# Optimization experiments

Measured on AMD Instinct MI355X. Metric: run time of the kernel, lower is better.

The kernel has to match this reference:

```python
import jax, jax.numpy as jnp
import numpy as np

N_ATOMS = 300000
N_COLS = 8
VOCAB = 4096      # nn.Embedding(4096, per_col_dim)
D_COL = 32        # per_col_dim
HID = 256         # hidden_size
N_BONDS = 320000
B_GRAPHS = 6000
ATOMS_PER_GRAPH = 50
STEPS = 3
SENTINEL = 999999999


def _linear_params(key, fan_in, fan_out):
    lim = 1.0 / np.sqrt(fan_in)
    kw, kb = jax.random.split(key)
    W = jax.random.uniform(kw, (fan_out, fan_in), minval=-lim, maxval=lim, dtype=jnp.float32)
    b = jax.random.uniform(kb, (fan_out,), minval=-lim, maxval=lim, dtype=jnp.float32)
    return W, b


def setup_inputs() -> dict:
    key = jax.random.key(0)
    ks = jax.random.split(key, 8)
    a_features = jax.random.randint(ks[0], (N_ATOMS, N_COLS), 0, VOCAB, dtype=jnp.int32)
    uv = jax.random.randint(ks[1], (N_BONDS, 2), 0, N_ATOMS, dtype=jnp.int32)
    bextra = jax.random.randint(ks[2], (N_BONDS, 1), 0, 16, dtype=jnp.int32)
    b_features = jnp.concatenate([uv, bextra], axis=1)
    # contiguous equal-length scopes: graph i owns atoms [i*50, i*50+50)
    starts = np.arange(B_GRAPHS, dtype=np.int32) * ATOMS_PER_GRAPH
    lengths = np.full(B_GRAPHS, ATOMS_PER_GRAPH, dtype=np.int32)
    a_scopes = jnp.asarray(np.stack([starts, lengths], axis=1))
    emb_weights = jax.random.normal(ks[3], (N_COLS, VOCAB, D_COL), dtype=jnp.float32) * 0.02
    W_in, b_in = _linear_params(ks[4], D_COL, HID)
    W_self, b_self = _linear_params(ks[5], HID, HID)
    W_neigh, b_neigh = _linear_params(ks[6], HID, HID)
    W_out, b_out = _linear_params(ks[7], HID, HID)
    return {
        'a_features': a_features, 'b_features': b_features, 'a_scopes': a_scopes,
        'emb_weights': emb_weights,
        'W_in': W_in, 'b_in': b_in,
        'W_self': W_self, 'b_self': b_self,
        'W_neigh': W_neigh, 'b_neigh': b_neigh,
        'W_out': W_out, 'b_out': b_out,
    }


def reference(a_features, b_features, a_scopes, emb_weights,
              W_in, b_in, W_self, b_self, W_neigh, b_neigh, W_out, b_out):
    # --- per-column embedding lookup, summed over columns ---
    idx = jnp.remainder(a_features, VOCAB)
    idx = jnp.where(a_features >= SENTINEL, 0, idx)          # sentinel -> index 0
    x = jnp.zeros((a_features.shape[0], D_COL), dtype=emb_weights.dtype)
    for c in range(N_COLS):                                   # fixed small loop over columns
        x = x + emb_weights[c][idx[:, c]]
    h = x @ W_in.T + b_in                                     # [N, HID]
    # --- undirected edges -> two directed edge lists ---
    u = b_features[:, 0]
    v = b_features[:, 1]
    src = jnp.concatenate([u, v], axis=0)
    dst = jnp.concatenate([v, u], axis=0)
    # --- message passing steps ---
    for _ in range(STEPS):
        agg = jnp.zeros_like(h).at[dst].add(h[src])           # scatter-add neighbor sum
        h = jax.nn.relu(h @ W_self.T + b_self + agg @ W_neigh.T + b_neigh)
    h = h @ W_out.T + b_out
    # --- per-graph mean pooling over contiguous scopes ---
    lengths = a_scopes[:, 1]
    seg_ids = jnp.repeat(jnp.arange(a_scopes.shape[0]), lengths,
                         total_repeat_length=h.shape[0])
    sums = jax.ops.segment_sum(h, seg_ids, num_segments=a_scopes.shape[0])
    denom = jnp.maximum(lengths, 1).astype(h.dtype)[:, None]
    return sums / denom
```

## Files before the change

kernel.cpp:

```cpp
#include <hip/hip_runtime.h>

#define NATOMS 300000
#define NCOLS 8
#define VOCABSZ 4096
#define DCOL 32
#define HIDDIM 256
#define NBONDS 320000
#define NGRAPHS 6000
#define NSTEPS 3

constexpr int MP = 300032;
constexpr int MTILES128 = MP / 128;
constexpr int HSTR = 2 * HIDDIM;
constexpr int XSTR = 2 * DCOL;

typedef _Float16 f16;
typedef _Float16 f16x8 __attribute__((ext_vector_type(8)));
typedef float f32x4 __attribute__((ext_vector_type(4)));

constexpr float LO_SCALE = 2048.0f;
constexpr float INV_LO   = 1.0f / 2048.0f;

__device__ __forceinline__ void split2(float x, f16& h, f16& l) {
    h = (f16)x;
    l = (f16)((x - (float)h) * LO_SCALE);
}

__device__ __forceinline__ int swz(int row, int q) {
    return (row * 4 + (q ^ ((row >> 1) & 3))) * 8;
}

__device__ __forceinline__ void dma16(const f16* g, f16* l) {
    __builtin_amdgcn_global_load_lds(
        (const __attribute__((address_space(1))) uint32_t*)g,
        (__attribute__((address_space(3))) uint32_t*)l, 16, 0, 0);
}

static void* g_pool = nullptr;
__attribute__((constructor)) static void alloc_pool() {
    void* p = nullptr;
    if (hipMalloc(&p, (size_t)1024 * 1024 * 1024) == hipSuccess) {
        hipMemset(p, 0, (size_t)1024 * 1024 * 1024);
        g_pool = p;
    }
}

__global__ void fill_kernel(float* out, float v, int n) {
    int i = blockIdx.x * blockDim.x + threadIdx.x;
    if (i < n) out[i] = v;
}

__global__ void build_edges_kernel(const int* __restrict__ bf, int* __restrict__ esrc,
                                   int* __restrict__ nxt, int* head) {
    int e = blockIdx.x * blockDim.x + threadIdx.x;
    if (e >= 2 * NBONDS) return;
    int src, dst;
    if (e < NBONDS) { src = bf[e * 3 + 0]; dst = bf[e * 3 + 1]; }
    else { int i = e - NBONDS; src = bf[i * 3 + 1]; dst = bf[i * 3 + 0]; }
    esrc[e] = src;
    nxt[e] = atomicExch(&head[dst], e);
}

__global__ void wsplit_kernel(const float* __restrict__ W, f16* __restrict__ Wh,
                              f16* __restrict__ Wl, int n) {
    int i = blockIdx.x * blockDim.x + threadIdx.x;
    if (i >= n) return;
    split2(W[i], Wh[i], Wl[i]);
}

__global__ void bsum_kernel(const float* __restrict__ a, const float* __restrict__ b,
                            float* __restrict__ o) {
    int i = threadIdx.x;
    o[i] = a[i] + b[i];
}

__global__ void embed_kernel(const int* __restrict__ af, const float* __restrict__ emb,
                             f16* __restrict__ x) {
    int gid = blockIdx.x * blockDim.x + threadIdx.x;
    int i = gid >> 5, k = gid & 31;
    if (i >= NATOMS) return;
    float s = 0.0f;
#pragma unroll
    for (int c = 0; c < NCOLS; c++) {
        int v = af[i * NCOLS + c];
        int idx = v & (VOCABSZ - 1);
        if (v >= 999999999) idx = 0;
        s += emb[((size_t)c * VOCABSZ + idx) * DCOL + k];
    }
    f16 hi, lo;
    split2(s, hi, lo);
    x[(size_t)i * XSTR + k] = hi;
    x[(size_t)i * XSTR + DCOL + k] = lo;
}

__global__ void agg_kernel(const f16* __restrict__ H, f16* __restrict__ G,
                           const int* __restrict__ head, const int* __restrict__ nxt,
                           const int* __restrict__ esrc) {
    int wid = (blockIdx.x * blockDim.x + threadIdx.x) >> 6;
    int lane = threadIdx.x & 63;
    if (wid >= NATOMS) return;
    float a0 = 0.f, a1 = 0.f, a2 = 0.f, a3 = 0.f,
          a4 = 0.f, a5 = 0.f, a6 = 0.f, a7 = 0.f;
    int e = head[wid];
    while (e >= 0) {
        int src = esrc[e];
        const f16x8 v = *(const f16x8*)(H + (size_t)src * HSTR + lane * 8);
        a0 += (float)v[0]; a1 += (float)v[1]; a2 += (float)v[2]; a3 += (float)v[3];
        a4 += (float)v[4]; a5 += (float)v[5]; a6 += (float)v[6]; a7 += (float)v[7];
        e = nxt[e];
    }
    const bool isLo = lane >= 32;
    if (isLo) {
        a0 *= INV_LO; a1 *= INV_LO; a2 *= INV_LO; a3 *= INV_LO;
        a4 *= INV_LO; a5 *= INV_LO; a6 *= INV_LO; a7 *= INV_LO;
    }
    float s0 = a0 + __shfl_xor(a0, 32, 64);
    float s1 = a1 + __shfl_xor(a1, 32, 64);
    float s2 = a2 + __shfl_xor(a2, 32, 64);
    float s3 = a3 + __shfl_xor(a3, 32, 64);
    float s4 = a4 + __shfl_xor(a4, 32, 64);
    float s5 = a5 + __shfl_xor(a5, 32, 64);
    float s6 = a6 + __shfl_xor(a6, 32, 64);
    float s7 = a7 + __shfl_xor(a7, 32, 64);
    f16x8 o;
#define EMIT(J, S)                                                    \
    {                                                                 \
        const f16 hv = (f16)(S);                                      \
        o[J] = isLo ? (f16)(((S) - (float)hv) * LO_SCALE) : hv;       \
    }
    EMIT(0, s0) EMIT(1, s1) EMIT(2, s2) EMIT(3, s3)
    EMIT(4, s4) EMIT(5, s5) EMIT(6, s6) EMIT(7, s7)
#undef EMIT
    *(f16x8*)(G + (size_t)wid * HSTR + lane * 8) = o;
}

template <bool HAS_A2, bool RELU, int K>
__global__ __launch_bounds__(512, 2) void mfma_gemm(
    const f16* __restrict__ A1, const f16* __restrict__ A2,
    const f16* __restrict__ B1h, const f16* __restrict__ B1l,
    const f16* __restrict__ B2h, const f16* __restrict__ B2l,
    const float* __restrict__ bias, f16* __restrict__ C) {
    constexpr int OAH = 0, OAL = 4096, OBH = 8192, OBL = 16384, BUFH = 24576;
    __shared__ __align__(16) f16 lds[2 * BUFH];

    const int t = threadIdx.x;
    const int m0 = blockIdx.x * 128;
    const int lane = t & 63;
    const int wid = t >> 6;
    const int wr = wid >> 2;
    const int wc = wid & 3;
    const int quad = lane >> 4;
    const int l16 = lane & 15;

    const int ra_ = wid * 16 + (lane >> 2);
    const int qs_ = (lane & 3) ^ ((ra_ >> 1) & 3);
    const int ko_ = qs_ * 8;

    f32x4 acch[4][4], accl[4][4];
#pragma unroll
    for (int a = 0; a < 4; a++)
#pragma unroll
        for (int b = 0; b < 4; b++) {
            acch[a][b] = (f32x4){0.f, 0.f, 0.f, 0.f};
            accl[a][b] = (f32x4){0.f, 0.f, 0.f, 0.f};
        }

    constexpr int NMAT = HAS_A2 ? 2 : 1;
    constexpr int NST = (K / 32) * NMAT;

#define ISSUE_STAGE(S, BUF)                                                    \
    {                                                                          \
        const int mat_ = HAS_A2 ? ((S) & 1) : 0;                               \
        const int kb_ = (HAS_A2 ? ((S) >> 1) : (S)) * 32;                      \
        const f16* A_ = (mat_ == 0) ? A1 : A2;                                 \
        const f16* Bh_ = (mat_ == 0) ? B1h : B2h;                              \
        const f16* Bl_ = (mat_ == 0) ? B1l : B2l;                              \
        f16* const dst_ = lds + (BUF) * BUFH + wid * 512;                      \
        const size_t arow_ = (size_t)(m0 + ra_) * (2 * K) + kb_ + ko_;         \
        dma16(A_ + arow_, dst_ + OAH);                                         \
        dma16(A_ + arow_ + K, dst_ + OAL);                                     \
        const size_t brow_ = (size_t)ra_ * K + kb_ + ko_;                      \
        dma16(Bh_ + brow_, dst_ + OBH);                                        \
        dma16(Bh_ + brow_ + (size_t)128 * K, dst_ + OBH + 4096);               \
        dma16(Bl_ + brow_, dst_ + OBL);                                        \
        dma16(Bl_ + brow_ + (size_t)128 * K, dst_ + OBL + 4096);               \
    }

    ISSUE_STAGE(0, 0);

    for (int s = 0; s < NST; s++) {
        __syncthreads();
        if (s + 1 < NST) ISSUE_STAGE(s + 1, (s + 1) & 1);

        const f16* cb = lds + (s & 1) * BUFH;
        const f16* sAh = cb + OAH;
        const f16* sAl = cb + OAL;
        const f16* sBh = cb + OBH;
        const f16* sBl = cb + OBL;

        f16x8 fah[4], fal[4];
#pragma unroll
        for (int mt = 0; mt < 4; mt++) {
            const int src = swz(wr * 64 + mt * 16 + l16, quad);
            fah[mt] = *(const f16x8*)(sAh + src);
            fal[mt] = *(const f16x8*)(sAl + src);
        }
#pragma unroll
        for (int nt = 0; nt < 4; nt++) {
            const int src = swz(wc * 64 + nt * 16 + l16, quad);
            const f16x8 bh = *(const f16x8*)(sBh + src);
            const f16x8 bl = *(const f16x8*)(sBl + src);
#pragma unroll
            for (int mt = 0; mt < 4; mt++) {
                acch[mt][nt] = __builtin_amdgcn_mfma_f32_16x16x32_f16(fah[mt], bh, acch[mt][nt], 0, 0, 0);
                accl[mt][nt] = __builtin_amdgcn_mfma_f32_16x16x32_f16(fah[mt], bl, accl[mt][nt], 0, 0, 0);
                accl[mt][nt] = __builtin_amdgcn_mfma_f32_16x16x32_f16(fal[mt], bh, accl[mt][nt], 0, 0, 0);
            }
        }
    }
#undef ISSUE_STAGE

#pragma unroll
    for (int mt = 0; mt < 4; mt++) {
#pragma unroll
        for (int nt = 0; nt < 4; nt++) {
            const int col = wc * 64 + nt * 16 + l16;
            const float bv = bias[col];
#pragma unroll
            for (int r = 0; r < 4; r++) {
                const int row = m0 + wr * 64 + mt * 16 + quad * 4 + r;
                float v = acch[mt][nt][r] + accl[mt][nt][r] * INV_LO + bv;
                if (RELU) v = fmaxf(v, 0.f);
                f16 hi, lo;
                split2(v, hi, lo);
                C[(size_t)row * HSTR + col] = hi;
                C[(size_t)row * HSTR + HIDDIM + col] = lo;
            }
        }
    }
}

__global__ void readout_mean_kernel(const f16* __restrict__ H,
                                    const int* __restrict__ scopes, float* __restrict__ G) {
    int g = blockIdx.x;
    int n = threadIdx.x;
    int start = scopes[g * 2 + 0];
    int len = scopes[g * 2 + 1];
    float s = 0.f;
    for (int j = 0; j < len; j++) {
        const f16* row = H + (size_t)(start + j) * HSTR;
        s += (float)row[n] + (float)row[HIDDIM + n] * INV_LO;
    }
    int d = len > 1 ? len : 1;
    G[(size_t)g * HIDDIM + n] = s / (float)d;
}

__global__ __launch_bounds__(256) void out_gemm_kernel(
    const float* __restrict__ G, const float* __restrict__ W,
    const float* __restrict__ bias, float* __restrict__ out) {
    __shared__ float sG[16 * 256];
    const int g0 = blockIdx.x * 16;
    const int t = threadIdx.x;
#pragma unroll
    for (int i = 0; i < 16; i++) sG[i * 256 + t] = G[(size_t)(g0 + i) * 256 + t];
    __syncthreads();
    const float bv = bias[t];
    const float* wrow = W + (size_t)t * 256;
    float acc[16];
#pragma unroll
    for (int g = 0; g < 16; g++) acc[g] = 0.f;
    for (int k = 0; k < 256; k += 4) {
        const float4 w = *(const float4*)(wrow + k);
#pragma unroll
        for (int g = 0; g < 16; g++) {
            const float4 a = *(const float4*)(sG + g * 256 + k);
            acc[g] = fmaf(a.x, w.x, acc[g]);
            acc[g] = fmaf(a.y, w.y, acc[g]);
            acc[g] = fmaf(a.z, w.z, acc[g]);
            acc[g] = fmaf(a.w, w.w, acc[g]);
        }
    }
#pragma unroll
    for (int g = 0; g < 16; g++) out[(size_t)(g0 + g) * 256 + t] = acc[g] + bv;
}

extern "C" void kernel_launch(void* const* d_in, const int* in_sizes, int n_in,
                              void* d_out, int out_size, void* d_ws, size_t ws_size,
                              hipStream_t stream) {
    const int* a_features = (const int*)d_in[0];
    const int* b_features = (const int*)d_in[1];
    const int* a_scopes   = (const int*)d_in[2];
    const float* emb      = (const float*)d_in[3];
    const float* W_in     = (const float*)d_in[4];
    const float* b_in     = (const float*)d_in[5];
    const float* W_self   = (const float*)d_in[6];
    const float* b_self   = (const float*)d_in[7];
    const float* W_neigh  = (const float*)d_in[8];
    const float* b_neigh  = (const float*)d_in[9];
    const float* W_out    = (const float*)d_in[10];
    const float* b_out    = (const float*)d_in[11];

    if (g_pool == nullptr) {
        fill_kernel<<<(out_size + 255) / 256, 256, 0, stream>>>(
            (float*)d_out, 77777.0f, out_size);
        return;
    }

    f16* p = (f16*)g_pool;
    const size_t HB2 = (size_t)MP * HSTR;
    f16* bufA = p;
    f16* bufB = p + HB2;
    f16* bufC = p + 2 * HB2;
    f16* xbuf = p + 3 * HB2;
    f16* Winh = xbuf + (size_t)MP * XSTR;
    f16* Winl = Winh + HIDDIM * DCOL;
    f16* Wsh  = Winl + HIDDIM * DCOL;
    f16* Wsl  = Wsh + HIDDIM * HIDDIM;
    f16* Wnh  = Wsl + HIDDIM * HIDDIM;
    f16* Wnl  = Wnh + HIDDIM * HIDDIM;
    float* Gmean = (float*)(Wnl + HIDDIM * HIDDIM);
    float* bsum  = Gmean + (size_t)NGRAPHS * HIDDIM;
    int* esrc = (int*)(bsum + HIDDIM);
    int* nxt  = esrc + 2 * NBONDS;
    int* head = nxt + 2 * NBONDS;

    constexpr int NPAD = MP - NATOMS;

    hipMemsetAsync(head, 0xFF, (size_t)MP * sizeof(int), stream);
    build_edges_kernel<<<(2 * NBONDS + 255) / 256, 256, 0, stream>>>(b_features, esrc, nxt, head);
    wsplit_kernel<<<(HIDDIM * DCOL + 255) / 256, 256, 0, stream>>>(W_in, Winh, Winl, HIDDIM * DCOL);
    wsplit_kernel<<<(HIDDIM * HIDDIM + 255) / 256, 256, 0, stream>>>(W_self, Wsh, Wsl, HIDDIM * HIDDIM);
    wsplit_kernel<<<(HIDDIM * HIDDIM + 255) / 256, 256, 0, stream>>>(W_neigh, Wnh, Wnl, HIDDIM * HIDDIM);
    bsum_kernel<<<1, HIDDIM, 0, stream>>>(b_self, b_neigh, bsum);

    constexpr int PADH = NPAD * HSTR / 2;
    fill_kernel<<<(PADH + 255) / 256, 256, 0, stream>>>((float*)(bufA + (size_t)NATOMS * HSTR), 0.f, PADH);
    fill_kernel<<<(PADH + 255) / 256, 256, 0, stream>>>((float*)(bufB + (size_t)NATOMS * HSTR), 0.f, PADH);
    fill_kernel<<<(PADH + 255) / 256, 256, 0, stream>>>((float*)(bufC + (size_t)NATOMS * HSTR), 0.f, PADH);
    constexpr int PADX = NPAD * XSTR / 2;
    fill_kernel<<<(PADX + 255) / 256, 256, 0, stream>>>((float*)(xbuf + (size_t)NATOMS * XSTR), 0.f, PADX);

    embed_kernel<<<(NATOMS * DCOL + 255) / 256, 256, 0, stream>>>(a_features, emb, xbuf);
    mfma_gemm<false, false, DCOL><<<MTILES128, 512, 0, stream>>>(
        xbuf, nullptr, Winh, Winl, nullptr, nullptr, b_in, bufA);

    f16* h  = bufA;
    f16* g  = bufB;
    f16* hn = bufC;
    for (int s = 0; s < NSTEPS; s++) {
        agg_kernel<<<NATOMS / 4, 256, 0, stream>>>(h, g, head, nxt, esrc);
        mfma_gemm<true, true, HIDDIM><<<MTILES128, 512, 0, stream>>>(
            h, g, Wsh, Wsl, Wnh, Wnl, bsum, hn);
        f16* old = h;
        h = hn; hn = g; g = old;
    }

    readout_mean_kernel<<<NGRAPHS, 256, 0, stream>>>(h, a_scopes, Gmean);
    out_gemm_kernel<<<NGRAPHS / 16, 256, 0, stream>>>(Gmean, W_out, b_out, (float*)d_out);
}
```

Before: 1.944 ms.

## Triple-buffer the LDS staging in the split-fp16 MFMA GEMM

The GEMM's LDS staging goes from two buffers to three, so global-to-LDS copies are issued two K-stages ahead instead of one. Each stage's copies are tracked with an explicit s_waitcnt vmcnt(6) and a raw s_barrier, replacing the plain __syncthreads, and a sched_barrier keeps the compiler from moving work across that point. The aim is to hide global load latency behind more MFMA work. The cost is LDS per block growing from 96KB to 144KB, which was already too large for two blocks per CU. It also relies on the hand-written wait count matching the six copies issued per stage.

```diff
diff --git a/kernel.cpp b/kernel.cpp
--- a/kernel.cpp
+++ b/kernel.cpp
@@ -141,7 +141,7 @@
     const f16* __restrict__ B2h, const f16* __restrict__ B2l,
     const float* __restrict__ bias, f16* __restrict__ C) {
     constexpr int OAH = 0, OAL = 4096, OBH = 8192, OBL = 16384, BUFH = 24576;
-    __shared__ __align__(16) f16 lds[2 * BUFH];
+    __shared__ __align__(16) f16 lds[3 * BUFH];
 
     const int t = threadIdx.x;
     const int m0 = blockIdx.x * 128;
@@ -186,39 +186,59 @@
         dma16(Bl_ + brow_ + (size_t)128 * K, dst_ + OBL + 4096);               \
     }
 
+#define COMPUTE_STAGE(BUF)                                                     \
+    {                                                                          \
+        const f16* cb = lds + (BUF) * BUFH;                                    \
+        const f16* sAh = cb + OAH;                                             \
+        const f16* sAl = cb + OAL;                                             \
+        const f16* sBh = cb + OBH;                                             \
+        const f16* sBl = cb + OBL;                                             \
+        f16x8 fah[4], fal[4];                                                  \
+        _Pragma("unroll")                                                      \
+        for (int mt = 0; mt < 4; mt++) {                                       \
+            const int src = swz(wr * 64 + mt * 16 + l16, quad);                \
+            fah[mt] = *(const f16x8*)(sAh + src);                              \
+            fal[mt] = *(const f16x8*)(sAl + src);                              \
+        }                                                                      \
+        _Pragma("unroll")                                                      \
+        for (int nt = 0; nt < 4; nt++) {                                       \
+            const int src = swz(wc * 64 + nt * 16 + l16, quad);                \
+            const f16x8 bh = *(const f16x8*)(sBh + src);                       \
+            const f16x8 bl = *(const f16x8*)(sBl + src);                       \
+            _Pragma("unroll")                                                  \
+            for (int mt = 0; mt < 4; mt++) {                                   \
+                acch[mt][nt] = __builtin_amdgcn_mfma_f32_16x16x32_f16(         \
+                    fah[mt], bh, acch[mt][nt], 0, 0, 0);                       \
+                accl[mt][nt] = __builtin_amdgcn_mfma_f32_16x16x32_f16(         \
+                    fah[mt], bl, accl[mt][nt], 0, 0, 0);                       \
+                accl[mt][nt] = __builtin_amdgcn_mfma_f32_16x16x32_f16(         \
+                    fal[mt], bh, accl[mt][nt], 0, 0, 0);                       \
+            }                                                                  \
+        }                                                                      \
+    }
+
     ISSUE_STAGE(0, 0);
-
-    for (int s = 0; s < NST; s++) {
-        __syncthreads();
-        if (s + 1 < NST) ISSUE_STAGE(s + 1, (s + 1) & 1);
-
-        const f16* cb = lds + (s & 1) * BUFH;
-        const f16* sAh = cb + OAH;
-        const f16* sAl = cb + OAL;
-        const f16* sBh = cb + OBH;
-        const f16* sBl = cb + OBL;
-
-        f16x8 fah[4], fal[4];
-#pragma unroll
-        for (int mt = 0; mt < 4; mt++) {
-            const int src = swz(wr * 64 + mt * 16 + l16, quad);
-            fah[mt] = *(const f16x8*)(sAh + src);
-            fal[mt] = *(const f16x8*)(sAl + src);
+    asm volatile("" ::: "memory");
+    if (NST > 1) ISSUE_STAGE(1, 1);
+
+    int buf = 0;
+    for (int s = 0; s < NST - 1; s++) {
+        asm volatile("s_waitcnt vmcnt(6) lgkmcnt(0)" ::: "memory");
+        __builtin_amdgcn_s_barrier();
+        __builtin_amdgcn_sched_barrier(0);
+        if (s + 2 < NST) {
+            int nb = buf + 2; if (nb >= 3) nb -= 3;
+            ISSUE_STAGE(s + 2, nb);
         }
-#pragma unroll
-        for (int nt = 0; nt < 4; nt++) {
-            const int src = swz(wc * 64 + nt * 16 + l16, quad);
-            const f16x8 bh = *(const f16x8*)(sBh + src);
-            const f16x8 bl = *(const f16x8*)(sBl + src);
-#pragma unroll
-            for (int mt = 0; mt < 4; mt++) {
-                acch[mt][nt] = __builtin_amdgcn_mfma_f32_16x16x32_f16(fah[mt], bh, acch[mt][nt], 0, 0, 0);
-                accl[mt][nt] = __builtin_amdgcn_mfma_f32_16x16x32_f16(fah[mt], bl, accl[mt][nt], 0, 0, 0);
-                accl[mt][nt] = __builtin_amdgcn_mfma_f32_16x16x32_f16(fal[mt], bh, accl[mt][nt], 0, 0, 0);
-            }
-        }
-    }
+        COMPUTE_STAGE(buf);
+        buf = (buf == 2) ? 0 : buf + 1;
+    }
+    asm volatile("s_waitcnt vmcnt(0) lgkmcnt(0)" ::: "memory");
+    __builtin_amdgcn_s_barrier();
+    __builtin_amdgcn_sched_barrier(0);
+    COMPUTE_STAGE(buf);
 #undef ISSUE_STAGE
+#undef COMPUTE_STAGE
 
 #pragma unroll
     for (int mt = 0; mt < 4; mt++) {
```

After: 1.925 ms. No clear change (-1.0%).
